# Performance work log

Measured on AMD Instinct MI355X. Metric: run time of the kernel, lower is better.

Reference implementation:

```python
import jax, jax.numpy as jnp
import numpy as np

DIM = 256
HEADS = 4
DIM_HEAD = 64
INNER = HEADS * DIM_HEAD  # 256
SCALE = DIM_HEAD ** -0.5


def setup_inputs() -> dict:
    key = jax.random.key(0)
    k1, k2, k3 = jax.random.split(key, 3)
    x = jax.random.normal(k1, (4, 4096, DIM), dtype=jnp.float32)
    # to_qkv: Linear(dim, inner*3, bias=False) -> weight [3*inner, dim]
    w_qkv = jax.random.normal(k2, (3 * INNER, DIM), dtype=jnp.float32) * (DIM ** -0.5)
    # to_out: Linear(inner, dim) with bias
    w_out = jax.random.normal(k3, (DIM, INNER), dtype=jnp.float32) * (INNER ** -0.5)
    b_out = jnp.zeros((DIM,), dtype=jnp.float32)
    return {"x": x, "w_qkv": w_qkv, "w_out": w_out, "b_out": b_out}


def reference(x, w_qkv, w_out, b_out):
    b, n, _ = x.shape
    qkv = x @ w_qkv.T                      # [b, n, 3*inner]
    q, k, v = jnp.split(qkv, 3, axis=-1)   # each [b, n, inner]

    def heads(t):
        return t.reshape(b, n, HEADS, DIM_HEAD).transpose(0, 2, 1, 3)  # [b, h, n, d]

    q, k, v = heads(q), heads(k), heads(v)
    dots = jnp.einsum('bhid,bhjd->bhij', q, k) * SCALE   # [b, h, n, n]
    attn = jax.nn.softmax(dots, axis=-1)
    out = jnp.einsum('bhij,bhjd->bhid', attn, v)         # [b, h, n, d]
    out = out.transpose(0, 2, 1, 3).reshape(b, n, INNER)  # [b, n, inner]
    return out @ w_out.T + b_out  # dropout p=0.0 -> identity
```

## Files before the change

kernel.cpp:

```cpp
#include <hip/hip_runtime.h>
#include <hip/hip_bf16.h>
#include <stdint.h>

typedef unsigned short ushort_t;
typedef __attribute__((ext_vector_type(8))) short short8;
typedef __attribute__((ext_vector_type(4))) ushort_t ushort4v;
typedef __attribute__((ext_vector_type(4))) float float4v;
typedef __attribute__((ext_vector_type(16))) float floatx16;

#define MFMA32(a, b, c) __builtin_amdgcn_mfma_f32_32x32x16_bf16(a, b, c, 0, 0, 0)

#define BATCH 4
#define SEQ 4096
#define DIM 256
#define HEADS 4
#define DHEAD 64
#define INNER 256
#define MROWS (BATCH * SEQ)
#define NQKV (3 * INNER)

__device__ __forceinline__ ushort_t f2bf(float f) {
    uint32_t u = __builtin_bit_cast(uint32_t, f);
    uint32_t r = (u + 0x7FFFu + ((u >> 16) & 1u)) >> 16;
    return (ushort_t)r;
}

__device__ __forceinline__ float exp2_fast(float x) {
#if __has_builtin(__builtin_amdgcn_exp2f)
    return __builtin_amdgcn_exp2f(x);
#else
    return exp2f(x);
#endif
}

__device__ __forceinline__ float max3f(float a, float b, float c) {
    return fmaxf(fmaxf(a, b), c);
}

__device__ __forceinline__ unsigned cvtpk_bf16(float lo, float hi) {
    unsigned r;
    asm("v_cvt_pk_bf16_f32 %0, %1, %2" : "=v"(r) : "v"(lo), "v"(hi));
    return r;
}

__device__ __forceinline__ void plswap(unsigned& a, unsigned& b) {
#if __has_builtin(__builtin_amdgcn_permlane32_swap)
    auto rr = __builtin_amdgcn_permlane32_swap(a, b, false, false);
    a = (unsigned)rr[0];
    b = (unsigned)rr[1];
#else
    unsigned sa = (unsigned)__shfl_xor((int)a, 32, 64);
    unsigned sb = (unsigned)__shfl_xor((int)b, 32, 64);
    bool upper = (threadIdx.x & 32) != 0;
    unsigned na = upper ? sb : a;
    unsigned nb = upper ? b : sa;
    a = na;
    b = nb;
#endif
}

__device__ __forceinline__ void gload_lds16(const ushort_t* g, ushort_t* l) {
    __builtin_amdgcn_global_load_lds(
        (__attribute__((address_space(1))) void*)(const_cast<ushort_t*>(g)),
        (__attribute__((address_space(3))) void*)l, 16, 0, 0);
}

__global__ __launch_bounds__(256) void convert_w(
    const float* __restrict__ wqkv, const float* __restrict__ wout,
    ushort_t* __restrict__ wqkvb, ushort_t* __restrict__ woutb) {
    const int NW = NQKV * DIM;
    const int NO = DIM * INNER;
    const float QS = 0.125f * 1.4426950408889634f;
    int idx = blockIdx.x * blockDim.x + threadIdx.x;
    int stride = gridDim.x * blockDim.x;
    for (int i = idx; i < NW + NO; i += stride) {
        if (i < NW) {
            float s = (i < INNER * DIM) ? QS : 1.0f;
            wqkvb[i] = f2bf(wqkv[i] * s);
        } else {
            int j = i - NW;
            woutb[j] = f2bf(wout[j]);
        }
    }
}

__global__ __launch_bounds__(256) void qkv_gemm(
    const float* __restrict__ X, const ushort_t* __restrict__ B,
    ushort_t* __restrict__ q, ushort_t* __restrict__ k, ushort_t* __restrict__ v) {
    __shared__ ushort_t Bs[128 * 256] __attribute__((aligned(16)));
    int bid = blockIdx.x;
    int swz = (bid & 7) * 96 + (bid >> 3);
    int mt = swz / 6, nb = swz % 6;
    int tid = threadIdx.x;
    int wid = tid >> 6, lane = tid & 63;
    const int l31 = lane & 31, hi = lane >> 5;

    const ushort_t* bsrc = B + (int64_t)nb * 128 * 256;
#pragma unroll
    for (int i = 0; i < 16; ++i) {
        int L = i * 256 + tid;
        int sl = L ^ ((L >> 5) & 31);
        gload_lds16(bsrc + (sl >> 5) * 256 + (sl & 31) * 8, &Bs[L * 8]);
    }

    int m0 = mt * 128 + wid * 32;
    const float* abase = X + (int64_t)(m0 + l31) * 256 + hi * 8;
    short8 af[16];
#pragma unroll
    for (int s = 0; s < 16; ++s) {
        float4v a0 = *(const float4v*)(abase + s * 16);
        float4v a1 = *(const float4v*)(abase + s * 16 + 4);
        union { unsigned u[4]; short8 s8; } fu;
        fu.u[0] = cvtpk_bf16(a0[0], a0[1]);
        fu.u[1] = cvtpk_bf16(a0[2], a0[3]);
        fu.u[2] = cvtpk_bf16(a1[0], a1[1]);
        fu.u[3] = cvtpk_bf16(a1[2], a1[3]);
        af[s] = fu.s8;
    }

    __syncthreads();

    floatx16 acc[4] = {};
    __builtin_amdgcn_s_setprio(1);
#pragma unroll
    for (int s = 0; s < 16; ++s) {
#pragma unroll
        for (int nt = 0; nt < 4; ++nt) {
            int n = nt * 32 + l31;
            int byte = (n * 512 + s * 32 + hi * 16) ^ ((n & 31) << 4);
            short8 bf = *(const short8*)((const char*)Bs + byte);
            acc[nt] = MFMA32(af[s], bf, acc[nt]);
        }
    }
    __builtin_amdgcn_s_setprio(0);

    int part = nb >> 1;
    if (part < 2) {
        ushort_t* dst = (part == 0) ? q : k;
#pragma unroll
        for (int nt = 0; nt < 4; ++nt) {
            int cc = (nb * 128 + nt * 32 + l31) & 255;
            int h = cc >> 6, d = cc & 63;
#pragma unroll
            for (int r = 0; r < 16; ++r) {
                int m = m0 + (r & 3) + 8 * (r >> 2) + 4 * hi;
                int bb = m >> 12, n = m & 4095;
                dst[((((int64_t)bb * HEADS + h) * SEQ) + n) * DHEAD + d] = f2bf(acc[nt][r]);
            }
        }
    } else {
#pragma unroll
        for (int nt = 0; nt < 4; ++nt) {
            int cc = (nb * 128 + nt * 32 + l31) & 255;
            int h = cc >> 6, d = cc & 63;
#pragma unroll
            for (int g = 0; g < 4; ++g) {
                int m = m0 + g * 8 + hi * 4;
                int bb = m >> 12, n = m & 4095;
                ushort4v pk;
#pragma unroll
                for (int r = 0; r < 4; ++r) pk[r] = f2bf(acc[nt][g * 4 + r]);
                *(ushort4v*)(v + ((((int64_t)bb * HEADS + h) * DHEAD) + d) * SEQ + n) = pk;
            }
        }
    }
}

__global__ __launch_bounds__(256, 2) void attn_kernel(
    const ushort_t* __restrict__ Qg, const ushort_t* __restrict__ Kg,
    const ushort_t* __restrict__ Vtg, ushort_t* __restrict__ Og) {
    int bid = blockIdx.x;
    int swz = (bid & 7) * 64 + (bid >> 3);
    int bh = swz >> 5;
    int qt = swz & 31;
    int tid = threadIdx.x;
    int wid = tid >> 6, lane = tid & 63;
    const int l31 = lane & 31;
    const int hi = lane >> 5;

    __shared__ ushort_t SM[2][16384] __attribute__((aligned(16)));

    const ushort_t* qbase = Qg + (int64_t)bh * SEQ * DHEAD;
    const ushort_t* kbase = Kg + (int64_t)bh * SEQ * DHEAD;
    const ushort_t* vtbase = Vtg + (int64_t)bh * DHEAD * SEQ;

    int q0 = qt * 128 + wid * 32;
    short8 qf[4];
#pragma unroll
    for (int s = 0; s < 4; ++s)
        qf[s] = *(const short8*)(qbase + (int64_t)(q0 + l31) * DHEAD + s * 16 + hi * 8);

    const ushort_t* kp[4];
    const ushort_t* vp[4];
    ushort_t* kld[4];
    ushort_t* vld[4];
#pragma unroll
    for (int jj = 0; jj < 4; ++jj) {
        int L = jj * 256 + tid;
        int sl = L ^ ((L >> 7) & 7);
        int s_ = sl >> 8, hi_ = (sl >> 7) & 1, key_ = sl & 127;
        kp[jj] = kbase + key_ * DHEAD + s_ * 16 + hi_ * 8;
        int ks_ = sl >> 7, hik_ = (sl >> 6) & 1, d_ = sl & 63;
        vp[jj] = vtbase + (int64_t)d_ * SEQ + ks_ * 16 + hik_ * 8;
        kld[jj] = &SM[0][(jj * 256 + wid * 64) * 8];
        vld[jj] = &SM[0][8192 + (jj * 256 + wid * 64) * 8];
    }

#define STAGE(BUF)                                           \
    {                                                        \
        _Pragma("unroll") for (int jj = 0; jj < 4; ++jj) {   \
            gload_lds16(kp[jj], kld[jj] + (BUF) * 16384);    \
            gload_lds16(vp[jj], vld[jj] + (BUF) * 16384);    \
            kp[jj] += 128 * DHEAD;                           \
            vp[jj] += 128;                                   \
        }                                                    \
    }

    int bS[4];
#pragma unroll
    for (int s = 0; s < 4; ++s) bS[s] = hi * 2048 + ((l31 * 16) ^ ((s * 2 + hi) << 4));
    const int tV = hi * 1024 + l31 * 16;

    floatx16 accO[2] = {};
    floatx16 mseed = {};
    float m_i = 0.f, l_i = 0.f;

    STAGE(0);
    __syncthreads();

    for (int it = 0; it < SEQ / 128; ++it) {
        int buf = it & 1;
        const char* smc = (const char*)SM + buf * 32768;
        const char* smv = smc + 16384;
        if (it < SEQ / 128 - 1) STAGE(buf ^ 1);

        floatx16 accS[4];
        __builtin_amdgcn_s_setprio(1);
#pragma unroll
        for (int s = 0; s < 4; ++s) {
#pragma unroll
            for (int kt = 0; kt < 4; ++kt) {
                short8 kf = *(const short8*)(smc + bS[s] + s * 4096 + kt * 512);
                accS[kt] = MFMA32(kf, qf[s], s == 0 ? mseed : accS[kt]);
            }
        }
        __builtin_amdgcn_s_setprio(0);

        float mk[4];
#pragma unroll
        for (int kt = 0; kt < 4; ++kt) {
            float t0 = max3f(accS[kt][0], accS[kt][1], accS[kt][2]);
            t0 = max3f(t0, accS[kt][3], accS[kt][4]);
            t0 = max3f(t0, accS[kt][5], accS[kt][6]);
            t0 = max3f(t0, accS[kt][7], accS[kt][8]);
            t0 = max3f(t0, accS[kt][9], accS[kt][10]);
            t0 = max3f(t0, accS[kt][11], accS[kt][12]);
            t0 = max3f(t0, accS[kt][13], accS[kt][14]);
            mk[kt] = fmaxf(t0, accS[kt][15]);
        }
        float mx = fmaxf(max3f(mk[0], mk[1], mk[2]), mk[3]);
        mx = fmaxf(mx, __shfl_xor(mx, 32, 64));

        if (!__all(mx <= 8.f)) {
            float mb = fmaxf(mx, 0.f);
            float corr = exp2_fast(-mb);
            l_i *= corr;
#pragma unroll
            for (int r = 0; r < 16; ++r) {
                int qr = (r & 3) + 8 * (r >> 2) + 4 * hi;
                float cr = __shfl(corr, qr, 64);
                accO[0][r] *= cr;
                accO[1][r] *= cr;
            }
            m_i += mb;
#pragma unroll
            for (int r = 0; r < 16; ++r) mseed[r] -= mb;
#pragma unroll
            for (int kt = 0; kt < 4; ++kt)
#pragma unroll
                for (int r = 0; r < 16; ++r) accS[kt][r] -= mb;
        }

        float rs0 = 0.f, rs1 = 0.f, rs2 = 0.f, rs3 = 0.f;
#pragma unroll
        for (int r = 0; r < 16; ++r) {
            float e0 = exp2_fast(accS[0][r]);
            float e1 = exp2_fast(accS[1][r]);
            float e2 = exp2_fast(accS[2][r]);
            float e3 = exp2_fast(accS[3][r]);
            accS[0][r] = e0;
            accS[1][r] = e1;
            accS[2][r] = e2;
            accS[3][r] = e3;
            rs0 += e0;
            rs1 += e1;
            rs2 += e2;
            rs3 += e3;
        }
        float rs = (rs0 + rs1) + (rs2 + rs3);
        rs += __shfl_xor(rs, 32, 64);
        l_i += rs;

        short8 pa[8];
#pragma unroll
        for (int kt = 0; kt < 4; ++kt) {
            unsigned w0 = cvtpk_bf16(accS[kt][0], accS[kt][1]);
            unsigned w1 = cvtpk_bf16(accS[kt][2], accS[kt][3]);
            unsigned w2 = cvtpk_bf16(accS[kt][4], accS[kt][5]);
            unsigned w3 = cvtpk_bf16(accS[kt][6], accS[kt][7]);
            unsigned w4 = cvtpk_bf16(accS[kt][8], accS[kt][9]);
            unsigned w5 = cvtpk_bf16(accS[kt][10], accS[kt][11]);
            unsigned w6 = cvtpk_bf16(accS[kt][12], accS[kt][13]);
            unsigned w7 = cvtpk_bf16(accS[kt][14], accS[kt][15]);
            plswap(w0, w2);
            plswap(w1, w3);
            plswap(w4, w6);
            plswap(w5, w7);
            union { unsigned u[4]; short8 s; } f0, f1;
            f0.u[0] = w0; f0.u[1] = w1; f0.u[2] = w2; f0.u[3] = w3;
            f1.u[0] = w4; f1.u[1] = w5; f1.u[2] = w6; f1.u[3] = w7;
            pa[2 * kt] = f0.s;
            pa[2 * kt + 1] = f1.s;
        }

        __builtin_amdgcn_s_setprio(1);
#pragma unroll
        for (int ks = 0; ks < 8; ++ks) {
            int va = tV ^ (ks << 4);
#pragma unroll
            for (int o = 0; o < 2; ++o) {
                short8 vf = *(const short8*)(smv + va + ks * 2048 + o * 512);
                accO[o] = MFMA32(pa[ks], vf, accO[o]);
            }
        }
        __builtin_amdgcn_s_setprio(0);

        __syncthreads();
    }

    int b = bh >> 2, h = bh & 3;
    float invl = 1.f / l_i;
#pragma unroll
    for (int r = 0; r < 16; ++r) {
        int qr = (r & 3) + 8 * (r >> 2) + 4 * hi;
        float inv = __shfl(invl, qr, 64);
        int n = q0 + qr;
#pragma unroll
        for (int o = 0; o < 2; ++o) {
            int d = o * 32 + l31;
            Og[((int64_t)b * SEQ + n) * INNER + h * 64 + d] = f2bf(accO[o][r] * inv);
        }
    }
#undef STAGE
}

__global__ __launch_bounds__(256) void proj_gemm(
    const ushort_t* __restrict__ A, const ushort_t* __restrict__ B,
    const float* __restrict__ bias, float* __restrict__ out) {
    __shared__ ushort_t Bs[128 * 256] __attribute__((aligned(16)));
    int bid = blockIdx.x;
    int swz = (bid & 7) * 64 + (bid >> 3);
    int mt = swz >> 1, nb = swz & 1;
    int tid = threadIdx.x;
    int wid = tid >> 6, lane = tid & 63;
    const int l31 = lane & 31, hi = lane >> 5;

    const ushort_t* bsrc = B + (int64_t)nb * 128 * 256;
#pragma unroll
    for (int i = 0; i < 16; ++i) {
        int L = i * 256 + tid;
        int sl = L ^ ((L >> 5) & 31);
        gload_lds16(bsrc + (sl >> 5) * 256 + (sl & 31) * 8, &Bs[L * 8]);
    }

    int m0 = mt * 64 + (wid & 1) * 32;
    int nside = wid >> 1;
    const ushort_t* abase = A + (int64_t)(m0 + l31) * 256 + hi * 8;
    short8 af[16];
#pragma unroll
    for (int s = 0; s < 16; ++s) af[s] = *(const short8*)(abase + s * 16);

    __syncthreads();

    floatx16 acc[2] = {};
    __builtin_amdgcn_s_setprio(1);
#pragma unroll
    for (int s = 0; s < 16; ++s) {
#pragma unroll
        for (int nt = 0; nt < 2; ++nt) {
            int n = nside * 64 + nt * 32 + l31;
            int byte = (n * 512 + s * 32 + hi * 16) ^ ((n & 31) << 4);
            short8 bf = *(const short8*)((const char*)Bs + byte);
            acc[nt] = MFMA32(af[s], bf, acc[nt]);
        }
    }
    __builtin_amdgcn_s_setprio(0);

#pragma unroll
    for (int nt = 0; nt < 2; ++nt) {
        int col = nb * 128 + nside * 64 + nt * 32 + l31;
        float bv = bias[col];
#pragma unroll
        for (int r = 0; r < 16; ++r) {
            int m = m0 + (r & 3) + 8 * (r >> 2) + 4 * hi;
            out[(int64_t)m * DIM + col] = acc[nt][r] + bv;
        }
    }
}

extern "C" void kernel_launch(void* const* d_in, const int* in_sizes, int n_in,
                              void* d_out, int out_size, void* d_ws, size_t ws_size,
                              hipStream_t stream) {
    const float* x = (const float*)d_in[0];
    const float* w_qkv = (const float*)d_in[1];
    const float* w_out = (const float*)d_in[2];
    const float* b_out = (const float*)d_in[3];
    float* out = (float*)d_out;

    ushort_t* ws = (ushort_t*)d_ws;
    const int64_t NW = (int64_t)NQKV * DIM;
    const int64_t NO = (int64_t)DIM * INNER;
    const int64_t NH = (int64_t)BATCH * HEADS * SEQ * DHEAD;
    ushort_t* wqkvb = ws;
    ushort_t* woutb = wqkvb + NW;
    ushort_t* qb = woutb + NO;
    ushort_t* kb = qb + NH;
    ushort_t* vb = kb + NH;
    ushort_t* ob = vb + NH;

    convert_w<<<256, 256, 0, stream>>>(w_qkv, w_out, wqkvb, woutb);
    qkv_gemm<<<768, 256, 0, stream>>>(x, wqkvb, qb, kb, vb);
    attn_kernel<<<512, 256, 0, stream>>>(qb, kb, vb, ob);
    proj_gemm<<<512, 256, 0, stream>>>(ob, woutb, b_out, out);
}
```

Before: 130.1 us.

## Software-pipeline attention loop: overlap QK of next tile with PV of current

Restructures the flash-attention inner loop so each iteration issues the QK^T MFMAs for tile i+1 back to back with the PV MFMAs for tile i. The softmax and packing then run while the next K/V stage loads, with explicit vmcnt waits and sched barriers around the syncthreads. The loop is manually unrolled by two to alternate buffers, with a prologue and an epilogue. The aim is to keep the matrix units busy across softmax, at the cost of more live registers (accS and pa carried across iterations) and extra barriers per tile.

```diff
diff --git a/kernel.cpp b/kernel.cpp
--- a/kernel.cpp
+++ b/kernel.cpp
@@ -223,120 +223,138 @@
 
     floatx16 accO[2] = {};
     floatx16 mseed = {};
-    float m_i = 0.f, l_i = 0.f;
+    float l_i = 0.f;
+    floatx16 accS[4];
+    short8 pa[8];
+
+#define QK_PHASE(SMC)                                                          \
+    {                                                                          \
+        _Pragma("unroll") for (int s = 0; s < 4; ++s) {                        \
+            _Pragma("unroll") for (int kt = 0; kt < 4; ++kt) {                 \
+                short8 kf = *(const short8*)((SMC) + bS[s] + s * 4096 + kt * 512); \
+                accS[kt] = MFMA32(kf, qf[s], s == 0 ? mseed : accS[kt]);       \
+            }                                                                  \
+        }                                                                      \
+    }
+
+#define PV_PHASE(SMV)                                                          \
+    {                                                                          \
+        _Pragma("unroll") for (int ks = 0; ks < 8; ++ks) {                     \
+            int va = tV ^ (ks << 4);                                           \
+            _Pragma("unroll") for (int o = 0; o < 2; ++o) {                    \
+                short8 vf = *(const short8*)((SMV) + va + ks * 2048 + o * 512);\
+                accO[o] = MFMA32(pa[ks], vf, accO[o]);                         \
+            }                                                                  \
+        }                                                                      \
+    }
+
+#define SOFTMAX_PACK()                                                         \
+    {                                                                          \
+        float mk[4];                                                           \
+        _Pragma("unroll") for (int kt = 0; kt < 4; ++kt) {                     \
+            float t0 = max3f(accS[kt][0], accS[kt][1], accS[kt][2]);           \
+            t0 = max3f(t0, accS[kt][3], accS[kt][4]);                          \
+            t0 = max3f(t0, accS[kt][5], accS[kt][6]);                          \
+            t0 = max3f(t0, accS[kt][7], accS[kt][8]);                          \
+            t0 = max3f(t0, accS[kt][9], accS[kt][10]);                         \
+            t0 = max3f(t0, accS[kt][11], accS[kt][12]);                        \
+            t0 = max3f(t0, accS[kt][13], accS[kt][14]);                        \
+            mk[kt] = fmaxf(t0, accS[kt][15]);                                  \
+        }                                                                      \
+        float mx = fmaxf(max3f(mk[0], mk[1], mk[2]), mk[3]);                   \
+        mx = fmaxf(mx, __shfl_xor(mx, 32, 64));                                \
+        if (!__all(mx <= 8.f)) {                                               \
+            float mb = fmaxf(mx, 0.f);                                         \
+            float corr = exp2_fast(-mb);                                       \
+            l_i *= corr;                                                       \
+            _Pragma("unroll") for (int r = 0; r < 16; ++r) {                   \
+                int qr = (r & 3) + 8 * (r >> 2) + 4 * hi;                      \
+                float cr = __shfl(corr, qr, 64);                               \
+                accO[0][r] *= cr;                                              \
+                accO[1][r] *= cr;                                              \
+            }                                                                  \
+            _Pragma("unroll") for (int r = 0; r < 16; ++r) mseed[r] -= mb;     \
+            _Pragma("unroll") for (int kt = 0; kt < 4; ++kt)                   \
+                _Pragma("unroll") for (int r = 0; r < 16; ++r)                 \
+                    accS[kt][r] -= mb;                                         \
+        }                                                                      \
+        float rs0 = 0.f, rs1 = 0.f, rs2 = 0.f, rs3 = 0.f;                      \
+        _Pragma("unroll") for (int r = 0; r < 16; ++r) {                       \
+            float e0 = exp2_fast(accS[0][r]);                                  \
+            float e1 = exp2_fast(accS[1][r]);                                  \
+            float e2 = exp2_fast(accS[2][r]);                                  \
+            float e3 = exp2_fast(accS[3][r]);                                  \
+            accS[0][r] = e0;                                                   \
+            accS[1][r] = e1;                                                   \
+            accS[2][r] = e2;                                                   \
+            accS[3][r] = e3;                                                   \
+            rs0 += e0;                                                         \
+            rs1 += e1;                                                         \
+            rs2 += e2;                                                         \
+            rs3 += e3;                                                         \
+        }                                                                      \
+        float rs = (rs0 + rs1) + (rs2 + rs3);                                  \
+        rs += __shfl_xor(rs, 32, 64);                                          \
+        l_i += rs;                                                             \
+        _Pragma("unroll") for (int kt = 0; kt < 4; ++kt) {                     \
+            unsigned w0 = cvtpk_bf16(accS[kt][0], accS[kt][1]);                \
+            unsigned w1 = cvtpk_bf16(accS[kt][2], accS[kt][3]);                \
+            unsigned w2 = cvtpk_bf16(accS[kt][4], accS[kt][5]);                \
+            unsigned w3 = cvtpk_bf16(accS[kt][6], accS[kt][7]);                \
+            unsigned w4 = cvtpk_bf16(accS[kt][8], accS[kt][9]);                \
+            unsigned w5 = cvtpk_bf16(accS[kt][10], accS[kt][11]);              \
+            unsigned w6 = cvtpk_bf16(accS[kt][12], accS[kt][13]);              \
+            unsigned w7 = cvtpk_bf16(accS[kt][14], accS[kt][15]);              \
+            plswap(w0, w2);                                                    \
+            plswap(w1, w3);                                                    \
+            plswap(w4, w6);                                                    \
+            plswap(w5, w7);                                                    \
+            union { unsigned u[4]; short8 s; } f0, f1;                         \
+            f0.u[0] = w0; f0.u[1] = w1; f0.u[2] = w2; f0.u[3] = w3;            \
+            f1.u[0] = w4; f1.u[1] = w5; f1.u[2] = w6; f1.u[3] = w7;            \
+            pa[2 * kt] = f0.s;                                                 \
+            pa[2 * kt + 1] = f1.s;                                             \
+        }                                                                      \
+    }
+
+#define VMFENCE()                                                              \
+    asm volatile("s_waitcnt vmcnt(0)" ::: "memory");                           \
+    __builtin_amdgcn_sched_barrier(0)
+
+#define SBAR()                                                                 \
+    __builtin_amdgcn_sched_barrier(0);                                         \
+    __syncthreads();                                                           \
+    __builtin_amdgcn_sched_barrier(0)
+
+#define ITER(SMC_OFF, SMV_OFF, SBUF, DO_STAGE)                                 \
+    {                                                                          \
+        __builtin_amdgcn_s_setprio(1);                                         \
+        QK_PHASE((const char*)SM + (SMC_OFF));                                 \
+        PV_PHASE((const char*)SM + (SMV_OFF));                                 \
+        __builtin_amdgcn_s_setprio(0);                                         \
+        SBAR();                       \
+        if (DO_STAGE) { STAGE(SBUF); }                                         \
+        SOFTMAX_PACK();                                                        \
+        VMFENCE();                                \
+        SBAR();                          \
+    }
 
     STAGE(0);
-    __syncthreads();
-
-    for (int it = 0; it < SEQ / 128; ++it) {
-        int buf = it & 1;
-        const char* smc = (const char*)SM + buf * 32768;
-        const char* smv = smc + 16384;
-        if (it < SEQ / 128 - 1) STAGE(buf ^ 1);
-
-        floatx16 accS[4];
-        __builtin_amdgcn_s_setprio(1);
-#pragma unroll
-        for (int s = 0; s < 4; ++s) {
-#pragma unroll
-            for (int kt = 0; kt < 4; ++kt) {
-                short8 kf = *(const short8*)(smc + bS[s] + s * 4096 + kt * 512);
-                accS[kt] = MFMA32(kf, qf[s], s == 0 ? mseed : accS[kt]);
-            }
-        }
-        __builtin_amdgcn_s_setprio(0);
-
-        float mk[4];
-#pragma unroll
-        for (int kt = 0; kt < 4; ++kt) {
-            float t0 = max3f(accS[kt][0], accS[kt][1], accS[kt][2]);
-            t0 = max3f(t0, accS[kt][3], accS[kt][4]);
-            t0 = max3f(t0, accS[kt][5], accS[kt][6]);
-            t0 = max3f(t0, accS[kt][7], accS[kt][8]);
-            t0 = max3f(t0, accS[kt][9], accS[kt][10]);
-            t0 = max3f(t0, accS[kt][11], accS[kt][12]);
-            t0 = max3f(t0, accS[kt][13], accS[kt][14]);
-            mk[kt] = fmaxf(t0, accS[kt][15]);
-        }
-        float mx = fmaxf(max3f(mk[0], mk[1], mk[2]), mk[3]);
-        mx = fmaxf(mx, __shfl_xor(mx, 32, 64));
-
-        if (!__all(mx <= 8.f)) {
-            float mb = fmaxf(mx, 0.f);
-            float corr = exp2_fast(-mb);
-            l_i *= corr;
-#pragma unroll
-            for (int r = 0; r < 16; ++r) {
-                int qr = (r & 3) + 8 * (r >> 2) + 4 * hi;
-                float cr = __shfl(corr, qr, 64);
-                accO[0][r] *= cr;
-                accO[1][r] *= cr;
-            }
-            m_i += mb;
-#pragma unroll
-            for (int r = 0; r < 16; ++r) mseed[r] -= mb;
-#pragma unroll
-            for (int kt = 0; kt < 4; ++kt)
-#pragma unroll
-                for (int r = 0; r < 16; ++r) accS[kt][r] -= mb;
-        }
-
-        float rs0 = 0.f, rs1 = 0.f, rs2 = 0.f, rs3 = 0.f;
-#pragma unroll
-        for (int r = 0; r < 16; ++r) {
-            float e0 = exp2_fast(accS[0][r]);
-            float e1 = exp2_fast(accS[1][r]);
-            float e2 = exp2_fast(accS[2][r]);
-            float e3 = exp2_fast(accS[3][r]);
-            accS[0][r] = e0;
-            accS[1][r] = e1;
-            accS[2][r] = e2;
-            accS[3][r] = e3;
-            rs0 += e0;
-            rs1 += e1;
-            rs2 += e2;
-            rs3 += e3;
-        }
-        float rs = (rs0 + rs1) + (rs2 + rs3);
-        rs += __shfl_xor(rs, 32, 64);
-        l_i += rs;
-
-        short8 pa[8];
-#pragma unroll
-        for (int kt = 0; kt < 4; ++kt) {
-            unsigned w0 = cvtpk_bf16(accS[kt][0], accS[kt][1]);
-            unsigned w1 = cvtpk_bf16(accS[kt][2], accS[kt][3]);
-            unsigned w2 = cvtpk_bf16(accS[kt][4], accS[kt][5]);
-            unsigned w3 = cvtpk_bf16(accS[kt][6], accS[kt][7]);
-            unsigned w4 = cvtpk_bf16(accS[kt][8], accS[kt][9]);
-            unsigned w5 = cvtpk_bf16(accS[kt][10], accS[kt][11]);
-            unsigned w6 = cvtpk_bf16(accS[kt][12], accS[kt][13]);
-            unsigned w7 = cvtpk_bf16(accS[kt][14], accS[kt][15]);
-            plswap(w0, w2);
-            plswap(w1, w3);
-            plswap(w4, w6);
-            plswap(w5, w7);
-            union { unsigned u[4]; short8 s; } f0, f1;
-            f0.u[0] = w0; f0.u[1] = w1; f0.u[2] = w2; f0.u[3] = w3;
-            f1.u[0] = w4; f1.u[1] = w5; f1.u[2] = w6; f1.u[3] = w7;
-            pa[2 * kt] = f0.s;
-            pa[2 * kt + 1] = f1.s;
-        }
-
-        __builtin_amdgcn_s_setprio(1);
-#pragma unroll
-        for (int ks = 0; ks < 8; ++ks) {
-            int va = tV ^ (ks << 4);
-#pragma unroll
-            for (int o = 0; o < 2; ++o) {
-                short8 vf = *(const short8*)(smv + va + ks * 2048 + o * 512);
-                accO[o] = MFMA32(pa[ks], vf, accO[o]);
-            }
-        }
-        __builtin_amdgcn_s_setprio(0);
-
-        __syncthreads();
-    }
+    VMFENCE();
+    SBAR();
+    STAGE(1);
+    QK_PHASE((const char*)SM);
+    SOFTMAX_PACK();
+    VMFENCE();
+    SBAR();
+
+#pragma unroll 1
+    for (int p = 0; p < 15; ++p) {
+        ITER(32768, 16384, 0, true);
+        ITER(0, 32768 + 16384, 1, true);
+    }
+    ITER(32768, 16384, 0, false);
+    PV_PHASE((const char*)SM + 32768 + 16384);
 
     int b = bh >> 2, h = bh & 3;
     float invl = 1.f / l_i;
@@ -352,6 +370,12 @@
         }
     }
 #undef STAGE
+#undef QK_PHASE
+#undef PV_PHASE
+#undef SOFTMAX_PACK
+#undef VMFENCE
+#undef SBAR
+#undef ITER
 }
 
 __global__ __launch_bounds__(256) void proj_gemm(
```

Result: faster. 126.8 us (-2.5%).

## Split attention KV range in two halves with separate merge kernel

Applied to the files above, without the earlier changes.

Each query tile's key/value range is split across two blocks (flash-decoding style), doubling the grid to 1024 blocks and halving the KV tile to 64 keys, which lets occupancy rise to 4 blocks per CU. Each half writes unnormalised fp32 partial outputs plus running max and sum, and a new merge kernel combines the two with rescaling and writes the bf16 output. This targets the small original grid of 512 blocks on a 256-CU device. In exchange it adds fp32 partial traffic, an extra launch, and shorter inner loops with more per-iteration overhead.

```diff
diff --git a/kernel.cpp b/kernel.cpp
--- a/kernel.cpp
+++ b/kernel.cpp
@@ -6,6 +6,7 @@
 typedef __attribute__((ext_vector_type(8))) short short8;
 typedef __attribute__((ext_vector_type(4))) ushort_t ushort4v;
 typedef __attribute__((ext_vector_type(4))) float float4v;
+typedef __attribute__((ext_vector_type(2))) float floatx2;
 typedef __attribute__((ext_vector_type(16))) float floatx16;
 
 #define MFMA32(a, b, c) __builtin_amdgcn_mfma_f32_32x32x16_bf16(a, b, c, 0, 0, 0)
@@ -166,23 +167,26 @@
     }
 }
 
-__global__ __launch_bounds__(256, 2) void attn_kernel(
+__global__ __launch_bounds__(256, 4) void attn_kernel(
     const ushort_t* __restrict__ Qg, const ushort_t* __restrict__ Kg,
-    const ushort_t* __restrict__ Vtg, ushort_t* __restrict__ Og) {
+    const ushort_t* __restrict__ Vtg, float* __restrict__ opart,
+    float* __restrict__ mlout) {
     int bid = blockIdx.x;
-    int swz = (bid & 7) * 64 + (bid >> 3);
-    int bh = swz >> 5;
-    int qt = swz & 31;
+    int swz = (bid & 7) * 128 + (bid >> 3);
+    int bh = swz >> 6;
+    int qt = (swz >> 1) & 31;
+    int half = swz & 1;
     int tid = threadIdx.x;
     int wid = tid >> 6, lane = tid & 63;
     const int l31 = lane & 31;
     const int hi = lane >> 5;
 
-    __shared__ ushort_t SM[2][16384] __attribute__((aligned(16)));
+    __shared__ ushort_t SM[2][8192] __attribute__((aligned(16)));
 
     const ushort_t* qbase = Qg + (int64_t)bh * SEQ * DHEAD;
     const ushort_t* kbase = Kg + (int64_t)bh * SEQ * DHEAD;
     const ushort_t* vtbase = Vtg + (int64_t)bh * DHEAD * SEQ;
+    const int kv0 = half * 2048;
 
     int q0 = qt * 128 + wid * 32;
     short8 qf[4];
@@ -190,36 +194,30 @@
     for (int s = 0; s < 4; ++s)
         qf[s] = *(const short8*)(qbase + (int64_t)(q0 + l31) * DHEAD + s * 16 + hi * 8);
 
-    const ushort_t* kp[4];
-    const ushort_t* vp[4];
-    ushort_t* kld[4];
-    ushort_t* vld[4];
-#pragma unroll
-    for (int jj = 0; jj < 4; ++jj) {
+    const ushort_t* kp[2];
+    const ushort_t* vp[2];
+    ushort_t* kld[2];
+    ushort_t* vld[2];
+#pragma unroll
+    for (int jj = 0; jj < 2; ++jj) {
         int L = jj * 256 + tid;
-        int sl = L ^ ((L >> 7) & 7);
-        int s_ = sl >> 8, hi_ = (sl >> 7) & 1, key_ = sl & 127;
-        kp[jj] = kbase + key_ * DHEAD + s_ * 16 + hi_ * 8;
-        int ks_ = sl >> 7, hik_ = (sl >> 6) & 1, d_ = sl & 63;
-        vp[jj] = vtbase + (int64_t)d_ * SEQ + ks_ * 16 + hik_ * 8;
+        int sl = L ^ ((L >> 6) & 7);
+        int s_ = sl >> 7, hi_ = (sl >> 6) & 1, low = sl & 63;
+        kp[jj] = kbase + (int64_t)(kv0 + low) * DHEAD + s_ * 16 + hi_ * 8;
+        vp[jj] = vtbase + (int64_t)low * SEQ + kv0 + s_ * 16 + hi_ * 8;
         kld[jj] = &SM[0][(jj * 256 + wid * 64) * 8];
-        vld[jj] = &SM[0][8192 + (jj * 256 + wid * 64) * 8];
-    }
-
-#define STAGE(BUF)                                           \
-    {                                                        \
-        _Pragma("unroll") for (int jj = 0; jj < 4; ++jj) {   \
-            gload_lds16(kp[jj], kld[jj] + (BUF) * 16384);    \
-            gload_lds16(vp[jj], vld[jj] + (BUF) * 16384);    \
-            kp[jj] += 128 * DHEAD;                           \
-            vp[jj] += 128;                                   \
-        }                                                    \
-    }
-
-    int bS[4];
-#pragma unroll
-    for (int s = 0; s < 4; ++s) bS[s] = hi * 2048 + ((l31 * 16) ^ ((s * 2 + hi) << 4));
-    const int tV = hi * 1024 + l31 * 16;
+        vld[jj] = &SM[0][4096 + (jj * 256 + wid * 64) * 8];
+    }
+
+#define STAGE(BUF)                                          \
+    {                                                       \
+        _Pragma("unroll") for (int jj = 0; jj < 2; ++jj) {  \
+            gload_lds16(kp[jj], kld[jj] + (BUF) * 8192);    \
+            gload_lds16(vp[jj], vld[jj] + (BUF) * 8192);    \
+            kp[jj] += 64 * DHEAD;                           \
+            vp[jj] += 64;                                   \
+        }                                                   \
+    }
 
     floatx16 accO[2] = {};
     floatx16 mseed = {};
@@ -228,27 +226,28 @@
     STAGE(0);
     __syncthreads();
 
-    for (int it = 0; it < SEQ / 128; ++it) {
+    for (int it = 0; it < 32; ++it) {
         int buf = it & 1;
-        const char* smc = (const char*)SM + buf * 32768;
-        const char* smv = smc + 16384;
-        if (it < SEQ / 128 - 1) STAGE(buf ^ 1);
-
-        floatx16 accS[4];
+        const char* smc = (const char*)SM + buf * 16384;
+        const char* smv = smc + 8192;
+        if (it < 31) STAGE(buf ^ 1);
+
+        floatx16 accS[2];
         __builtin_amdgcn_s_setprio(1);
 #pragma unroll
         for (int s = 0; s < 4; ++s) {
-#pragma unroll
-            for (int kt = 0; kt < 4; ++kt) {
-                short8 kf = *(const short8*)(smc + bS[s] + s * 4096 + kt * 512);
+            int bSs = hi * 1024 + ((l31 * 16) ^ ((s * 2 + hi) << 4)) + s * 2048;
+#pragma unroll
+            for (int kt = 0; kt < 2; ++kt) {
+                short8 kf = *(const short8*)(smc + bSs + kt * 512);
                 accS[kt] = MFMA32(kf, qf[s], s == 0 ? mseed : accS[kt]);
             }
         }
         __builtin_amdgcn_s_setprio(0);
 
-        float mk[4];
-#pragma unroll
-        for (int kt = 0; kt < 4; ++kt) {
+        float mk[2];
+#pragma unroll
+        for (int kt = 0; kt < 2; ++kt) {
             float t0 = max3f(accS[kt][0], accS[kt][1], accS[kt][2]);
             t0 = max3f(t0, accS[kt][3], accS[kt][4]);
             t0 = max3f(t0, accS[kt][5], accS[kt][6]);
@@ -258,7 +257,7 @@
             t0 = max3f(t0, accS[kt][13], accS[kt][14]);
             mk[kt] = fmaxf(t0, accS[kt][15]);
         }
-        float mx = fmaxf(max3f(mk[0], mk[1], mk[2]), mk[3]);
+        float mx = fmaxf(mk[0], mk[1]);
         mx = fmaxf(mx, __shfl_xor(mx, 32, 64));
 
         if (!__all(mx <= 8.f)) {
@@ -276,34 +275,28 @@
 #pragma unroll
             for (int r = 0; r < 16; ++r) mseed[r] -= mb;
 #pragma unroll
-            for (int kt = 0; kt < 4; ++kt)
+            for (int kt = 0; kt < 2; ++kt)
 #pragma unroll
                 for (int r = 0; r < 16; ++r) accS[kt][r] -= mb;
         }
 
-        float rs0 = 0.f, rs1 = 0.f, rs2 = 0.f, rs3 = 0.f;
+        float rs0 = 0.f, rs1 = 0.f;
 #pragma unroll
         for (int r = 0; r < 16; ++r) {
             float e0 = exp2_fast(accS[0][r]);
             float e1 = exp2_fast(accS[1][r]);
-            float e2 = exp2_fast(accS[2][r]);
-            float e3 = exp2_fast(accS[3][r]);
             accS[0][r] = e0;
             accS[1][r] = e1;
-            accS[2][r] = e2;
-            accS[3][r] = e3;
             rs0 += e0;
             rs1 += e1;
-            rs2 += e2;
-            rs3 += e3;
-        }
-        float rs = (rs0 + rs1) + (rs2 + rs3);
+        }
+        float rs = rs0 + rs1;
         rs += __shfl_xor(rs, 32, 64);
         l_i += rs;
 
-        short8 pa[8];
-#pragma unroll
-        for (int kt = 0; kt < 4; ++kt) {
+        short8 pa[4];
+#pragma unroll
+        for (int kt = 0; kt < 2; ++kt) {
             unsigned w0 = cvtpk_bf16(accS[kt][0], accS[kt][1]);
             unsigned w1 = cvtpk_bf16(accS[kt][2], accS[kt][3]);
             unsigned w2 = cvtpk_bf16(accS[kt][4], accS[kt][5]);
@@ -325,11 +318,11 @@
 
         __builtin_amdgcn_s_setprio(1);
 #pragma unroll
-        for (int ks = 0; ks < 8; ++ks) {
-            int va = tV ^ (ks << 4);
+        for (int ks = 0; ks < 4; ++ks) {
+            int va = ks * 2048 + hi * 1024 + ((l31 ^ (ks * 2 + hi)) << 4);
 #pragma unroll
             for (int o = 0; o < 2; ++o) {
-                short8 vf = *(const short8*)(smv + va + ks * 2048 + o * 512);
+                short8 vf = *(const short8*)(smv + va + o * 512);
                 accO[o] = MFMA32(pa[ks], vf, accO[o]);
             }
         }
@@ -338,20 +331,55 @@
         __syncthreads();
     }
 
-    int b = bh >> 2, h = bh & 3;
-    float invl = 1.f / l_i;
+    float* ob2 = opart + (int64_t)(half * 16 + bh) * SEQ * 64;
 #pragma unroll
     for (int r = 0; r < 16; ++r) {
         int qr = (r & 3) + 8 * (r >> 2) + 4 * hi;
-        float inv = __shfl(invl, qr, 64);
         int n = q0 + qr;
 #pragma unroll
         for (int o = 0; o < 2; ++o) {
-            int d = o * 32 + l31;
-            Og[((int64_t)b * SEQ + n) * INNER + h * 64 + d] = f2bf(accO[o][r] * inv);
-        }
+            ob2[(int64_t)n * 64 + o * 32 + l31] = accO[o][r];
+        }
+    }
+    if (hi == 0) {
+        floatx2 mlv;
+        mlv[0] = m_i;
+        mlv[1] = l_i;
+        *(floatx2*)(mlout + ((int64_t)(half * 16 + bh) * SEQ + q0 + l31) * 2) = mlv;
     }
 #undef STAGE
+}
+
+__global__ __launch_bounds__(256) void merge_kernel(
+    const float* __restrict__ opart, const float* __restrict__ ml,
+    ushort_t* __restrict__ ob) {
+    int f = blockIdx.x * 256 + threadIdx.x;
+    int d8 = f & 7;
+    int n = (f >> 3) & 4095;
+    int bh = f >> 15;
+
+    const float* mlp0 = ml + ((int64_t)bh * SEQ + n) * 2;
+    const float* mlp1 = ml + ((int64_t)(16 + bh) * SEQ + n) * 2;
+    float m0 = mlp0[0], l0 = mlp0[1];
+    float m1 = mlp1[0], l1 = mlp1[1];
+    float m = fmaxf(m0, m1);
+    float e0 = exp2_fast(m0 - m), e1 = exp2_fast(m1 - m);
+    float inv = 1.f / (l0 * e0 + l1 * e1);
+    float c0 = e0 * inv, c1 = e1 * inv;
+
+    const float4v* p0 = (const float4v*)(opart + ((int64_t)bh * SEQ + n) * 64 + d8 * 8);
+    const float4v* p1 = (const float4v*)(opart + ((int64_t)(16 + bh) * SEQ + n) * 64 + d8 * 8);
+    float4v a0 = p0[0], a1 = p0[1];
+    float4v b0 = p1[0], b1 = p1[1];
+
+    union { unsigned u[4]; short8 s8; } fu;
+    fu.u[0] = cvtpk_bf16(c0 * a0[0] + c1 * b0[0], c0 * a0[1] + c1 * b0[1]);
+    fu.u[1] = cvtpk_bf16(c0 * a0[2] + c1 * b0[2], c0 * a0[3] + c1 * b0[3]);
+    fu.u[2] = cvtpk_bf16(c0 * a1[0] + c1 * b1[0], c0 * a1[1] + c1 * b1[1]);
+    fu.u[3] = cvtpk_bf16(c0 * a1[2] + c1 * b1[2], c0 * a1[3] + c1 * b1[3]);
+
+    int b = bh >> 2, h = bh & 3;
+    *(short8*)(ob + ((int64_t)b * SEQ + n) * INNER + h * 64 + d8 * 8) = fu.s8;
 }
 
 __global__ __launch_bounds__(256) void proj_gemm(
@@ -427,9 +455,12 @@
     ushort_t* kb = qb + NH;
     ushort_t* vb = kb + NH;
     ushort_t* ob = vb + NH;
+    float* opart = (float*)(ob + NH);
+    float* mlbuf = opart + (int64_t)2 * 16 * SEQ * 64;
 
     convert_w<<<256, 256, 0, stream>>>(w_qkv, w_out, wqkvb, woutb);
     qkv_gemm<<<768, 256, 0, stream>>>(x, wqkvb, qb, kb, vb);
-    attn_kernel<<<512, 256, 0, stream>>>(qb, kb, vb, ob);
+    attn_kernel<<<1024, 256, 0, stream>>>(qb, kb, vb, opart, mlbuf);
+    merge_kernel<<<2048, 256, 0, stream>>>(opart, mlbuf, ob);
     proj_gemm<<<512, 256, 0, stream>>>(ob, woutb, b_out, out);
 }
```

New measurement: 176.6 us. +35.7%, slower.
